# Performance work log

Measured on AMD Instinct MI355X. Metric: run time of the kernel, lower is better.

## Reference

```python
import jax, jax.numpy as jnp
import numpy as np

EMB = 16
N_LEFT = 100000
N_RIGHT = 100000
N_EDGES = 3200000


def setup_inputs() -> dict:
    key = jax.random.key(0)
    ks = jax.random.split(key, 16)
    s = 1.0 / np.sqrt(EMB)
    inp = {
        "left_features": jax.random.normal(ks[0], (N_LEFT, EMB), jnp.float32),
        "edge_indices": jax.random.randint(ks[1], (2, N_EDGES), 0, N_RIGHT, jnp.int64) if jax.config.jax_enable_x64 else jax.random.randint(ks[1], (2, N_EDGES), 0, N_RIGHT, jnp.int32),
        "edge_features": jax.random.normal(ks[2], (N_EDGES, 1), jnp.float32),
        "right_features": jax.random.normal(ks[3], (N_RIGHT, EMB), jnp.float32),
        # feature_module_left: Linear(emb, emb, bias=True)
        "W_left": jax.random.uniform(ks[4], (EMB, EMB), jnp.float32, -s, s),
        "b_left": jax.random.uniform(ks[5], (EMB,), jnp.float32, -s, s),
        # feature_module_edge: Linear(1, emb, bias=False)
        "W_edge": jax.random.uniform(ks[6], (1, EMB), jnp.float32, -1.0, 1.0),
        # feature_module_right: Linear(emb, emb, bias=False)
        "W_right": jax.random.uniform(ks[7], (EMB, EMB), jnp.float32, -s, s),
        # feature_module_final: ReLU -> Linear(emb, emb)
        "W_final": jax.random.uniform(ks[8], (EMB, EMB), jnp.float32, -s, s),
        "b_final": jax.random.uniform(ks[9], (EMB,), jnp.float32, -s, s),
        # post_conv_module: ReLU -> Linear(emb, emb)
        "W_post": jax.random.uniform(ks[10], (EMB, EMB), jnp.float32, -s, s),
        "b_post": jax.random.uniform(ks[11], (EMB,), jnp.float32, -s, s),
        # output_module: Linear(2*emb, emb) -> ReLU -> Linear(emb, emb)
        "W_out1": jax.random.uniform(ks[12], (2 * EMB, EMB), jnp.float32, -1.0 / np.sqrt(2 * EMB), 1.0 / np.sqrt(2 * EMB)),
        "b_out1": jax.random.uniform(ks[13], (EMB,), jnp.float32, -s, s),
        "W_out2": jax.random.uniform(ks[14], (EMB, EMB), jnp.float32, -s, s),
        "b_out2": jax.random.uniform(ks[15], (EMB,), jnp.float32, -s, s),
    }
    return inp


def reference(left_features, edge_indices, edge_features, right_features,
              W_left, b_left, W_edge, W_right, W_final, b_final,
              W_post, b_post, W_out1, b_out1, W_out2, b_out2):
    left_idx = edge_indices[0]
    right_idx = edge_indices[1]
    n_right = right_features.shape[0]

    # per-edge messages: [E, emb]
    msg_left = left_features[left_idx] @ W_left + b_left
    msg_edge = edge_features @ W_edge
    msg_right = right_features[right_idx] @ W_right
    messages = jax.nn.relu(msg_left + msg_edge + msg_right) @ W_final + b_final

    # scatter-add over right nodes
    aggregated = jax.ops.segment_sum(messages, right_idx, num_segments=n_right)

    post = jax.nn.relu(aggregated) @ W_post + b_post
    h = jnp.concatenate([post, right_features], axis=-1)  # [N_right, 2*emb]
    out = jax.nn.relu(h @ W_out1 + b_out1) @ W_out2 + b_out2
    return out
```

## Files before the change

### kernel.cpp

```cpp
#include <hip/hip_runtime.h>

#define EMB 16
#define NPB 196
#define BNODES 256
#define MAXNB 512
#define PCHUNK 6656
#define RPTC 13
#define MAXCHUNKS 512
#define REC_CAP 2048
#define RPT 4
typedef unsigned int u32;
typedef unsigned long long u64;

__global__ void zero_f32(float* __restrict__ p, size_t n) {
    size_t i = (size_t)blockIdx.x * blockDim.x + threadIdx.x;
    size_t stride = (size_t)gridDim.x * blockDim.x;
    for (; i < n; i += stride) p[i] = 0.0f;
}

__global__ void zero_i32(int* __restrict__ p, int n) {
    int i = blockIdx.x * blockDim.x + threadIdx.x;
    if (i < n) p[i] = 0;
}

__device__ __forceinline__ u32 bf16bits_rne(float x) {
    u32 u = __float_as_uint(x);
    return (u + 0x7fffu + ((u >> 16) & 1u)) >> 16;
}

__global__ void linear16_pack_kernel(const float* __restrict__ X, const float* __restrict__ W,
                                     const float* __restrict__ b, u32* __restrict__ Y, int N) {
    int tid = blockIdx.x * blockDim.x + threadIdx.x;
    int row = tid >> 3;
    int h = tid & 7;
    if (row >= N) return;
    float a0 = b ? b[h] : 0.0f;
    float a1 = b ? b[h + 8] : 0.0f;
    const float* xr = X + (size_t)row * EMB;
#pragma unroll
    for (int k = 0; k < EMB; ++k) {
        float xv = xr[k];
        a0 = fmaf(xv, W[k * EMB + h], a0);
        a1 = fmaf(xv, W[k * EMB + h + 8], a1);
    }
    Y[(size_t)row * 8 + h] = (bf16bits_rne(a1) << 16) | bf16bits_rne(a0);
}

__global__ void linear16_kernel(const float* __restrict__ X, const float* __restrict__ W,
                                const float* __restrict__ b, float* __restrict__ Y, int N) {
    int tid = blockIdx.x * blockDim.x + threadIdx.x;
    int row = tid >> 4;
    int j = tid & 15;
    if (row >= N) return;
    float acc = b ? b[j] : 0.0f;
    const float* xr = X + (size_t)row * EMB;
#pragma unroll
    for (int k = 0; k < EMB; ++k) acc = fmaf(xr[k], W[k * EMB + j], acc);
    Y[(size_t)row * EMB + j] = acc;
}

__launch_bounds__(512)
__global__ void chunk_sort_kernel(const int* __restrict__ eidx, const float* __restrict__ ef,
                                  u64* __restrict__ rec, int* __restrict__ cntM,
                                  int* __restrict__ cbaseM, int E, int NB) {
    __shared__ u64 srec[PCHUNK];
    __shared__ int hist[MAXNB];
    __shared__ int wsum[8];
    int t = threadIdx.x;
    int lane = t & 63, wid = t >> 6;
    int c = blockIdx.x;
    long long base = (long long)c * PCHUNK;
    int n = (int)(((long long)E - base) < PCHUNK ? ((long long)E - base) : PCHUNK);
    const int* ridx = eidx + E;

    for (int i = t; i < NB; i += 512) hist[i] = 0;
    __syncthreads();
    u64 rcv[RPTC];
    int pk[RPTC];
#pragma unroll
    for (int k = 0; k < RPTC; ++k) {
        int i = t + k * 512;
        rcv[k] = 0; pk[k] = 0;
        if (i < n) {
            int r = ridx[base + i];
            int l = eidx[base + i];
            float f = ef[base + i];
            int bb = r / NPB;
            int rl = r - bb * NPB;
            int rank = atomicAdd(&hist[bb], 1);
            rcv[k] = ((u64)__float_as_uint(f) << 32) | ((u64)(u32)l << 8) | (u32)rl;
            pk[k] = (bb << 13) | rank;
        }
    }
    __syncthreads();
    int v = (t < NB) ? hist[t] : 0;
    int inc = v;
#pragma unroll
    for (int d = 1; d < 64; d <<= 1) {
        int x = __shfl_up(inc, d, 64);
        if (lane >= d) inc += x;
    }
    if (lane == 63) wsum[wid] = inc;
    __syncthreads();
    int off = 0;
#pragma unroll
    for (int w = 0; w < 8; ++w) off += (w < wid) ? wsum[w] : 0;
    int ex = off + inc - v;
    if (t < NB) {
        cntM[(size_t)c * NB + t] = v;
        cbaseM[(size_t)c * NB + t] = ex;
        hist[t] = ex;
    }
    __syncthreads();
#pragma unroll
    for (int k = 0; k < RPTC; ++k) {
        int i = t + k * 512;
        if (i < n) srec[hist[pk[k] >> 13] + (pk[k] & 8191)] = rcv[k];
    }
    __syncthreads();
    for (int i = t; i < n; i += 512) rec[base + i] = srec[i];
}

__launch_bounds__(512)
__global__ void bucket_gather_kernel(const u64* __restrict__ rec, const int* __restrict__ cntM,
                                     const int* __restrict__ cbaseM,
                                     const u32* __restrict__ Lpk, const u32* __restrict__ Rpk,
                                     const float* __restrict__ We, const float* __restrict__ rf,
                                     const float* __restrict__ Wf, const float* __restrict__ bf,
                                     const float* __restrict__ Wp, const float* __restrict__ bp,
                                     const float* __restrict__ Wo1, const float* __restrict__ bo1,
                                     const float* __restrict__ Wo2, const float* __restrict__ bo2,
                                     float* __restrict__ out,
                                     int n_right, int NB, int nchunks) {
    __shared__ u64 srec[REC_CAP];
    __shared__ u32 addrtab[REC_CAP];
    __shared__ int runsum[MAXCHUNKS + 1];
    __shared__ int rbase[MAXCHUNKS];
    __shared__ int hist[BNODES], base_[BNODES];
    __shared__ int wsum[8];
    __shared__ float sWf[256], sWp[256], sWo1[512], sWo2[256], sb[64];
    int b = blockIdx.x;
    int t = threadIdx.x;
    int lane = t & 63, wid = t >> 6;
    int node0 = b * NPB;

    if (t < 256) { sWf[t] = Wf[t]; sWp[t] = Wp[t]; sWo2[t] = Wo2[t]; }
    sWo1[t] = Wo1[t];
    if (t < 16) { sb[t] = bf[t]; sb[16 + t] = bp[t]; sb[32 + t] = bo1[t]; sb[48 + t] = bo2[t]; }

    int len = (t < nchunks) ? cntM[(size_t)t * NB + b] : 0;
    int inc = len;
#pragma unroll
    for (int d = 1; d < 64; d <<= 1) {
        int x = __shfl_up(inc, d, 64);
        if (lane >= d) inc += x;
    }
    if (lane == 63) wsum[wid] = inc;
    __syncthreads();
    int off = 0;
#pragma unroll
    for (int w = 0; w < 8; ++w) off += (w < wid) ? wsum[w] : 0;
    int pexcl = off + inc - len;
    if (t < nchunks) { runsum[t] = pexcl; rbase[t] = t * PCHUNK + cbaseM[(size_t)t * NB + b]; }
    if (t == 511) runsum[nchunks] = off + inc;
    __syncthreads();
    int total = runsum[nchunks];

    int n = t >> 1, q = t & 1;
    int node = node0 + n;
    bool nv = (n < NPB) && (node < n_right);

    float we[16];
#pragma unroll
    for (int j = 0; j < 16; ++j) we[j] = We[j];

    float rv[16];
    if (nv) {
        const uint4* rp = (const uint4*)(Rpk + (size_t)node * 8);
        uint4 ra = rp[0], rb = rp[1];
        u32 w0 = ra.x, w1 = ra.y, w2 = ra.z, w3 = ra.w;
        u32 w4 = rb.x, w5 = rb.y, w6 = rb.z, w7 = rb.w;
        rv[0] = __uint_as_float(w0 << 16); rv[8]  = __uint_as_float(w0 & 0xffff0000u);
        rv[1] = __uint_as_float(w1 << 16); rv[9]  = __uint_as_float(w1 & 0xffff0000u);
        rv[2] = __uint_as_float(w2 << 16); rv[10] = __uint_as_float(w2 & 0xffff0000u);
        rv[3] = __uint_as_float(w3 << 16); rv[11] = __uint_as_float(w3 & 0xffff0000u);
        rv[4] = __uint_as_float(w4 << 16); rv[12] = __uint_as_float(w4 & 0xffff0000u);
        rv[5] = __uint_as_float(w5 << 16); rv[13] = __uint_as_float(w5 & 0xffff0000u);
        rv[6] = __uint_as_float(w6 << 16); rv[14] = __uint_as_float(w6 & 0xffff0000u);
        rv[7] = __uint_as_float(w7 << 16); rv[15] = __uint_as_float(w7 & 0xffff0000u);
    } else {
#pragma unroll
        for (int j = 0; j < 16; ++j) rv[j] = 0.0f;
    }

    float acc[16];
#pragma unroll
    for (int j = 0; j < 16; ++j) acc[j] = 0.0f;
    int dsum = 0;

    for (int tile0 = 0; tile0 < total; tile0 += REC_CAP) {
        int m = total - tile0; if (m > REC_CAP) m = REC_CAP;
        u64 rcl[RPT];
        int rnk[RPT];
        if (t < BNODES) hist[t] = 0;
        for (int r = t; r < nchunks; r += 512) {
            int g_lo = runsum[r], g_hi = runsum[r + 1];
            int lo = g_lo > tile0 ? g_lo : tile0;
            int hi = g_hi < tile0 + m ? g_hi : tile0 + m;
            int a = rbase[r] + (lo - g_lo);
            for (int g = lo; g < hi; ++g, ++a) addrtab[g - tile0] = (u32)a;
        }
        __syncthreads();
#pragma unroll
        for (int k = 0; k < RPT; ++k) {
            int i = t + k * 512;
            rcl[k] = (i < m) ? rec[(size_t)addrtab[i]] : 0;
        }
#pragma unroll
        for (int k = 0; k < RPT; ++k) {
            int i = t + k * 512;
            rnk[k] = (i < m) ? atomicAdd(&hist[(int)(rcl[k] & 0xffu)], 1) : 0;
        }
        __syncthreads();
        if (t < 64) {
            int h0 = hist[4 * t], h1 = hist[4 * t + 1], h2 = hist[4 * t + 2], h3 = hist[4 * t + 3];
            int s4 = h0 + h1 + h2 + h3;
            int inc4 = s4;
#pragma unroll
            for (int d = 1; d < 64; d <<= 1) {
                int x = __shfl_up(inc4, d, 64);
                if (t >= d) inc4 += x;
            }
            int ex = inc4 - s4;
            base_[4 * t] = ex;
            base_[4 * t + 1] = ex + h0;
            base_[4 * t + 2] = ex + h0 + h1;
            base_[4 * t + 3] = ex + h0 + h1 + h2;
        }
        __syncthreads();
#pragma unroll
        for (int k = 0; k < RPT; ++k) {
            int i = t + k * 512;
            if (i < m) srec[base_[(int)(rcl[k] & 0xffu)] + rnk[k]] = rcl[k];
        }
        __syncthreads();
        {
            int cc = nv ? hist[n] : 0;
            int b0_ = nv ? base_[n] : 0;
            if (q == 0) dsum += cc;
            for (int k = q; k < cc; k += 2) {
                u64 rc = srec[b0_ + k];
                int l = (int)((rc >> 8) & 0xFFFFFFu);
                float f = __uint_as_float((u32)(rc >> 32));
                const uint4* lp = (const uint4*)(Lpk + (size_t)l * 8);
                uint4 la = lp[0], lb = lp[1];
                u32 w0 = la.x, w1 = la.y, w2 = la.z, w3 = la.w;
                u32 w4 = lb.x, w5 = lb.y, w6 = lb.z, w7 = lb.w;
#define PAIR(h, lw) { \
                float l0 = __uint_as_float(lw << 16); \
                float l1 = __uint_as_float(lw & 0xffff0000u); \
                acc[h]     += fmaxf(fmaf(f, we[h], l0) + rv[h], 0.0f); \
                acc[h + 8] += fmaxf(fmaf(f, we[h + 8], l1) + rv[h + 8], 0.0f); }
                PAIR(0, w0) PAIR(1, w1) PAIR(2, w2) PAIR(3, w3)
                PAIR(4, w4) PAIR(5, w5) PAIR(6, w6) PAIR(7, w7)
#undef PAIR
            }
        }
        __syncthreads();
    }

#pragma unroll
    for (int j = 0; j < 16; ++j) acc[j] += __shfl_xor(acc[j], 1, 64);
    dsum += __shfl_xor(dsum, 1, 64);

    if (nv) {
        float rfx[16];
        const float4* Rf = (const float4*)(rf + (size_t)node * EMB);
#pragma unroll
        for (int k = 0; k < 4; ++k) {
            float4 w = Rf[k];
            rfx[4 * k] = w.x; rfx[4 * k + 1] = w.y; rfx[4 * k + 2] = w.z; rfx[4 * k + 3] = w.w;
        }
        float c = (float)dsum;
        float x[16], y[16], z[16], o[16];
#pragma unroll
        for (int j = 0; j < 16; ++j) {
            float a = c * sb[j];
#pragma unroll
            for (int k = 0; k < 16; ++k) a = fmaf(acc[k], sWf[k * 16 + j], a);
            x[j] = fmaxf(a, 0.0f);
        }
#pragma unroll
        for (int j = 0; j < 16; ++j) {
            float a = sb[16 + j];
#pragma unroll
            for (int k = 0; k < 16; ++k) a = fmaf(x[k], sWp[k * 16 + j], a);
            y[j] = a;
        }
#pragma unroll
        for (int j = 0; j < 16; ++j) {
            float a = sb[32 + j];
#pragma unroll
            for (int k = 0; k < 16; ++k) a = fmaf(y[k], sWo1[k * 16 + j], a);
#pragma unroll
            for (int k = 0; k < 16; ++k) a = fmaf(rfx[k], sWo1[(16 + k) * 16 + j], a);
            z[j] = fmaxf(a, 0.0f);
        }
#pragma unroll
        for (int j = 0; j < 16; ++j) {
            float a = sb[48 + j];
#pragma unroll
            for (int k = 0; k < 16; ++k) a = fmaf(z[k], sWo2[k * 16 + j], a);
            o[j] = a;
        }
        float4* Op = (float4*)(out + (size_t)node * EMB);
        Op[q * 2]     = make_float4(o[q * 8],     o[q * 8 + 1], o[q * 8 + 2], o[q * 8 + 3]);
        Op[q * 2 + 1] = make_float4(o[q * 8 + 4], o[q * 8 + 5], o[q * 8 + 6], o[q * 8 + 7]);
    }
}

__global__ void edge_kernel(const int* __restrict__ eidx, const float* __restrict__ ef,
                            const float* __restrict__ L, const float* __restrict__ R,
                            const float* __restrict__ We, float* __restrict__ S,
                            int* __restrict__ cnt, int E) {
    long long tid = (long long)blockIdx.x * blockDim.x + threadIdx.x;
    int e = (int)(tid >> 4);
    int j = (int)(tid & 15);
    if (e >= E) return;
    int l = eidx[e];
    int r = eidx[E + e];
    float v = L[(size_t)l * EMB + j] + ef[e] * We[j] + R[(size_t)r * EMB + j];
    v = fmaxf(v, 0.0f);
    unsafeAtomicAdd(&S[(size_t)r * EMB + j], v);
    if (j == 0) atomicAdd(&cnt[r], 1);
}

__global__ void final_kernel(const float* __restrict__ S, const int* __restrict__ deg,
                             const float* __restrict__ rf,
                             const float* __restrict__ Wf, const float* __restrict__ bf,
                             const float* __restrict__ Wp, const float* __restrict__ bp,
                             const float* __restrict__ Wo1, const float* __restrict__ bo1,
                             const float* __restrict__ Wo2, const float* __restrict__ bo2,
                             float* __restrict__ out, int N) {
    __shared__ float sWf[256], sWp[256], sWo1[512], sWo2[256];
    __shared__ float sb[64];
    int t = threadIdx.x;
    for (int i = t; i < 256; i += 256) { sWf[i] = Wf[i]; sWp[i] = Wp[i]; sWo2[i] = Wo2[i]; }
    for (int i = t; i < 512; i += 256) sWo1[i] = Wo1[i];
    if (t < 16) { sb[t] = bf[t]; sb[16 + t] = bp[t]; sb[32 + t] = bo1[t]; sb[48 + t] = bo2[t]; }
    __syncthreads();

    int r = blockIdx.x * blockDim.x + t;
    if (r >= N) return;

    float s[16], x[16], y[16], rv[16], z[16], o[16];
    const float4* Sp = (const float4*)(S + (size_t)r * EMB);
    const float4* Rp = (const float4*)(rf + (size_t)r * EMB);
#pragma unroll
    for (int k = 0; k < 4; ++k) {
        float4 v = Sp[k];
        s[4 * k] = v.x; s[4 * k + 1] = v.y; s[4 * k + 2] = v.z; s[4 * k + 3] = v.w;
        float4 w = Rp[k];
        rv[4 * k] = w.x; rv[4 * k + 1] = w.y; rv[4 * k + 2] = w.z; rv[4 * k + 3] = w.w;
    }
    float c = (float)deg[r];

#pragma unroll
    for (int j = 0; j < 16; ++j) {
        float a = c * sb[j];
#pragma unroll
        for (int k = 0; k < 16; ++k) a = fmaf(s[k], sWf[k * 16 + j], a);
        x[j] = fmaxf(a, 0.0f);
    }
#pragma unroll
    for (int j = 0; j < 16; ++j) {
        float a = sb[16 + j];
#pragma unroll
        for (int k = 0; k < 16; ++k) a = fmaf(x[k], sWp[k * 16 + j], a);
        y[j] = a;
    }
#pragma unroll
    for (int j = 0; j < 16; ++j) {
        float a = sb[32 + j];
#pragma unroll
        for (int k = 0; k < 16; ++k) a = fmaf(y[k], sWo1[k * 16 + j], a);
#pragma unroll
        for (int k = 0; k < 16; ++k) a = fmaf(rv[k], sWo1[(16 + k) * 16 + j], a);
        z[j] = fmaxf(a, 0.0f);
    }
#pragma unroll
    for (int j = 0; j < 16; ++j) {
        float a = sb[48 + j];
#pragma unroll
        for (int k = 0; k < 16; ++k) a = fmaf(z[k], sWo2[k * 16 + j], a);
        o[j] = a;
    }
    float4* Op = (float4*)(out + (size_t)r * EMB);
#pragma unroll
    for (int k = 0; k < 4; ++k)
        Op[k] = make_float4(o[4 * k], o[4 * k + 1], o[4 * k + 2], o[4 * k + 3]);
}

extern "C" void kernel_launch(void* const* d_in, const int* in_sizes, int n_in,
                              void* d_out, int out_size, void* d_ws, size_t ws_size,
                              hipStream_t stream) {
    const float* lf     = (const float*)d_in[0];
    const int*   eidx   = (const int*)d_in[1];
    const float* ef     = (const float*)d_in[2];
    const float* rf     = (const float*)d_in[3];
    const float* W_left = (const float*)d_in[4];
    const float* b_left = (const float*)d_in[5];
    const float* W_edge = (const float*)d_in[6];
    const float* W_right= (const float*)d_in[7];
    const float* W_final= (const float*)d_in[8];
    const float* b_final= (const float*)d_in[9];
    const float* W_post = (const float*)d_in[10];
    const float* b_post = (const float*)d_in[11];
    const float* W_out1 = (const float*)d_in[12];
    const float* b_out1 = (const float*)d_in[13];
    const float* W_out2 = (const float*)d_in[14];
    const float* b_out2 = (const float*)d_in[15];

    int n_left  = in_sizes[0] / EMB;
    int E       = in_sizes[2];
    int n_right = in_sizes[3] / EMB;
    float* out = (float*)d_out;

    int NB = (n_right + NPB - 1) / NPB;
    int nchunks = (E + PCHUNK - 1) / PCHUNK;

    size_t need = (size_t)E * 8
                + (size_t)nchunks * NB * 8
                + ((size_t)n_left + n_right) * 32;

    if (ws_size >= need && NB <= MAXNB && nchunks <= MAXCHUNKS) {
        u64* rec    = (u64*)d_ws;
        int* cntM   = (int*)(rec + (size_t)E);
        int* cbaseM = cntM + (size_t)nchunks * NB;
        u32* Lpk    = (u32*)(cbaseM + (size_t)nchunks * NB);
        u32* Rpk    = Lpk + (size_t)n_left * 8;

        linear16_pack_kernel<<<(n_left * 8 + 255) / 256, 256, 0, stream>>>(lf, W_left, b_left, Lpk, n_left);
        linear16_pack_kernel<<<(n_right * 8 + 255) / 256, 256, 0, stream>>>(rf, W_right, nullptr, Rpk, n_right);

        chunk_sort_kernel<<<nchunks, 512, 0, stream>>>(eidx, ef, rec, cntM, cbaseM, E, NB);

        bucket_gather_kernel<<<NB, 512, 0, stream>>>(rec, cntM, cbaseM, Lpk, Rpk, W_edge, rf,
                                                     W_final, b_final, W_post, b_post,
                                                     W_out1, b_out1, W_out2, b_out2,
                                                     out, n_right, NB, nchunks);
    } else {
        float* L   = (float*)d_ws;
        float* R   = L + (size_t)n_left * EMB;
        float* S   = R + (size_t)n_right * EMB;
        int*   cnt = (int*)(S + (size_t)n_right * EMB);

        zero_f32<<<2048, 256, 0, stream>>>(S, (size_t)n_right * EMB);
        zero_i32<<<(n_right + 255) / 256, 256, 0, stream>>>(cnt, n_right);

        linear16_kernel<<<(n_left * EMB + 255) / 256, 256, 0, stream>>>(lf, W_left, b_left, L, n_left);
        linear16_kernel<<<(n_right * EMB + 255) / 256, 256, 0, stream>>>(rf, W_right, nullptr, R, n_right);

        long long ethreads = (long long)E * EMB;
        edge_kernel<<<(unsigned)((ethreads + 255) / 256), 256, 0, stream>>>(eidx, ef, L, R, W_edge, S, cnt, E);

        final_kernel<<<(n_right + 255) / 256, 256, 0, stream>>>(S, cnt, rf,
            W_final, b_final, W_post, b_post, W_out1, b_out1, W_out2, b_out2, out, n_right);
    }
}
```

Baseline: 86.35 us.

## Halve nodes per bucket, use four threads per node, transpose chunk metadata

Buckets shrink from 196 to 98 right nodes, so the gather kernel launches about twice as many blocks (about 1021) and each node's edges are split across four threads instead of two, reduced with an extra xor shuffle. The chunk sort now scans two buckets per thread and writes count and base as a single int2 in bucket-major order, so each gather block reads its per-chunk metadata contiguously instead of with a stride. The aim is more parallelism in the gather and cheaper metadata reads. The cost is twice as much metadata written and each block doing the same per-chunk address-table setup over half as many edges.

```diff
diff --git a/kernel.cpp b/kernel.cpp
--- a/kernel.cpp
+++ b/kernel.cpp
@@ -1,9 +1,9 @@
 #include <hip/hip_runtime.h>
 
 #define EMB 16
-#define NPB 196
-#define BNODES 256
-#define MAXNB 512
+#define NPB 98
+#define NHIST 128
+#define MAXNB 1024
 #define PCHUNK 6656
 #define RPTC 13
 #define MAXCHUNKS 512
@@ -61,8 +61,8 @@
 
 __launch_bounds__(512)
 __global__ void chunk_sort_kernel(const int* __restrict__ eidx, const float* __restrict__ ef,
-                                  u64* __restrict__ rec, int* __restrict__ cntM,
-                                  int* __restrict__ cbaseM, int E, int NB) {
+                                  u64* __restrict__ rec, int2* __restrict__ cbM,
+                                  int E, int NB, int nchunks) {
     __shared__ u64 srec[PCHUNK];
     __shared__ int hist[MAXNB];
     __shared__ int wsum[8];
@@ -93,8 +93,11 @@
         }
     }
     __syncthreads();
-    int v = (t < NB) ? hist[t] : 0;
-    int inc = v;
+    int b0 = 2 * t, b1 = 2 * t + 1;
+    int v0 = (b0 < NB) ? hist[b0] : 0;
+    int v1 = (b1 < NB) ? hist[b1] : 0;
+    int s2 = v0 + v1;
+    int inc = s2;
 #pragma unroll
     for (int d = 1; d < 64; d <<= 1) {
         int x = __shfl_up(inc, d, 64);
@@ -105,12 +108,9 @@
     int off = 0;
 #pragma unroll
     for (int w = 0; w < 8; ++w) off += (w < wid) ? wsum[w] : 0;
-    int ex = off + inc - v;
-    if (t < NB) {
-        cntM[(size_t)c * NB + t] = v;
-        cbaseM[(size_t)c * NB + t] = ex;
-        hist[t] = ex;
-    }
+    int ex = off + inc - s2;
+    if (b0 < NB) { cbM[(size_t)b0 * nchunks + c] = make_int2(v0, ex);      hist[b0] = ex; }
+    if (b1 < NB) { cbM[(size_t)b1 * nchunks + c] = make_int2(v1, ex + v0); hist[b1] = ex + v0; }
     __syncthreads();
 #pragma unroll
     for (int k = 0; k < RPTC; ++k) {
@@ -122,8 +122,7 @@
 }
 
 __launch_bounds__(512)
-__global__ void bucket_gather_kernel(const u64* __restrict__ rec, const int* __restrict__ cntM,
-                                     const int* __restrict__ cbaseM,
+__global__ void bucket_gather_kernel(const u64* __restrict__ rec, const int2* __restrict__ cbM,
                                      const u32* __restrict__ Lpk, const u32* __restrict__ Rpk,
                                      const float* __restrict__ We, const float* __restrict__ rf,
                                      const float* __restrict__ Wf, const float* __restrict__ bf,
@@ -136,7 +135,7 @@
     __shared__ u32 addrtab[REC_CAP];
     __shared__ int runsum[MAXCHUNKS + 1];
     __shared__ int rbase[MAXCHUNKS];
-    __shared__ int hist[BNODES], base_[BNODES];
+    __shared__ int hist[NHIST], base_[NHIST];
     __shared__ int wsum[8];
     __shared__ float sWf[256], sWp[256], sWo1[512], sWo2[256], sb[64];
     int b = blockIdx.x;
@@ -148,7 +147,8 @@
     sWo1[t] = Wo1[t];
     if (t < 16) { sb[t] = bf[t]; sb[16 + t] = bp[t]; sb[32 + t] = bo1[t]; sb[48 + t] = bo2[t]; }
 
-    int len = (t < nchunks) ? cntM[(size_t)t * NB + b] : 0;
+    int len = 0, cb = 0;
+    if (t < nchunks) { int2 v = cbM[(size_t)b * nchunks + t]; len = v.x; cb = v.y; }
     int inc = len;
 #pragma unroll
     for (int d = 1; d < 64; d <<= 1) {
@@ -161,12 +161,12 @@
 #pragma unroll
     for (int w = 0; w < 8; ++w) off += (w < wid) ? wsum[w] : 0;
     int pexcl = off + inc - len;
-    if (t < nchunks) { runsum[t] = pexcl; rbase[t] = t * PCHUNK + cbaseM[(size_t)t * NB + b]; }
+    if (t < nchunks) { runsum[t] = pexcl; rbase[t] = t * PCHUNK + cb; }
     if (t == 511) runsum[nchunks] = off + inc;
     __syncthreads();
     int total = runsum[nchunks];
 
-    int n = t >> 1, q = t & 1;
+    int n = t >> 2, q = t & 3;
     int node = node0 + n;
     bool nv = (n < NPB) && (node < n_right);
 
@@ -202,7 +202,7 @@
         int m = total - tile0; if (m > REC_CAP) m = REC_CAP;
         u64 rcl[RPT];
         int rnk[RPT];
-        if (t < BNODES) hist[t] = 0;
+        if (t < NHIST) hist[t] = 0;
         for (int r = t; r < nchunks; r += 512) {
             int g_lo = runsum[r], g_hi = runsum[r + 1];
             int lo = g_lo > tile0 ? g_lo : tile0;
@@ -223,19 +223,17 @@
         }
         __syncthreads();
         if (t < 64) {
-            int h0 = hist[4 * t], h1 = hist[4 * t + 1], h2 = hist[4 * t + 2], h3 = hist[4 * t + 3];
-            int s4 = h0 + h1 + h2 + h3;
-            int inc4 = s4;
+            int h0 = hist[2 * t], h1 = hist[2 * t + 1];
+            int s2 = h0 + h1;
+            int inc2 = s2;
 #pragma unroll
             for (int d = 1; d < 64; d <<= 1) {
-                int x = __shfl_up(inc4, d, 64);
-                if (t >= d) inc4 += x;
+                int x = __shfl_up(inc2, d, 64);
+                if (t >= d) inc2 += x;
             }
-            int ex = inc4 - s4;
-            base_[4 * t] = ex;
-            base_[4 * t + 1] = ex + h0;
-            base_[4 * t + 2] = ex + h0 + h1;
-            base_[4 * t + 3] = ex + h0 + h1 + h2;
+            int ex = inc2 - s2;
+            base_[2 * t] = ex;
+            base_[2 * t + 1] = ex + h0;
         }
         __syncthreads();
 #pragma unroll
@@ -248,7 +246,7 @@
             int cc = nv ? hist[n] : 0;
             int b0_ = nv ? base_[n] : 0;
             if (q == 0) dsum += cc;
-            for (int k = q; k < cc; k += 2) {
+            for (int k = q; k < cc; k += 4) {
                 u64 rc = srec[b0_ + k];
                 int l = (int)((rc >> 8) & 0xFFFFFFu);
                 float f = __uint_as_float((u32)(rc >> 32));
@@ -270,8 +268,12 @@
     }
 
 #pragma unroll
-    for (int j = 0; j < 16; ++j) acc[j] += __shfl_xor(acc[j], 1, 64);
+    for (int j = 0; j < 16; ++j) {
+        acc[j] += __shfl_xor(acc[j], 1, 64);
+        acc[j] += __shfl_xor(acc[j], 2, 64);
+    }
     dsum += __shfl_xor(dsum, 1, 64);
+    dsum += __shfl_xor(dsum, 2, 64);
 
     if (nv) {
         float rfx[16];
@@ -314,8 +316,7 @@
             o[j] = a;
         }
         float4* Op = (float4*)(out + (size_t)node * EMB);
-        Op[q * 2]     = make_float4(o[q * 8],     o[q * 8 + 1], o[q * 8 + 2], o[q * 8 + 3]);
-        Op[q * 2 + 1] = make_float4(o[q * 8 + 4], o[q * 8 + 5], o[q * 8 + 6], o[q * 8 + 7]);
+        Op[q] = make_float4(o[q * 4], o[q * 4 + 1], o[q * 4 + 2], o[q * 4 + 3]);
     }
 }
 
@@ -430,22 +431,21 @@
     int nchunks = (E + PCHUNK - 1) / PCHUNK;
 
     size_t need = (size_t)E * 8
-                + (size_t)nchunks * NB * 8
+                + (size_t)NB * nchunks * 8
                 + ((size_t)n_left + n_right) * 32;
 
     if (ws_size >= need && NB <= MAXNB && nchunks <= MAXCHUNKS) {
-        u64* rec    = (u64*)d_ws;
-        int* cntM   = (int*)(rec + (size_t)E);
-        int* cbaseM = cntM + (size_t)nchunks * NB;
-        u32* Lpk    = (u32*)(cbaseM + (size_t)nchunks * NB);
-        u32* Rpk    = Lpk + (size_t)n_left * 8;
+        u64*  rec = (u64*)d_ws;
+        int2* cbM = (int2*)(rec + (size_t)E);
+        u32*  Lpk = (u32*)(cbM + (size_t)NB * nchunks);
+        u32*  Rpk = Lpk + (size_t)n_left * 8;
 
         linear16_pack_kernel<<<(n_left * 8 + 255) / 256, 256, 0, stream>>>(lf, W_left, b_left, Lpk, n_left);
         linear16_pack_kernel<<<(n_right * 8 + 255) / 256, 256, 0, stream>>>(rf, W_right, nullptr, Rpk, n_right);
 
-        chunk_sort_kernel<<<nchunks, 512, 0, stream>>>(eidx, ef, rec, cntM, cbaseM, E, NB);
-
-        bucket_gather_kernel<<<NB, 512, 0, stream>>>(rec, cntM, cbaseM, Lpk, Rpk, W_edge, rf,
+        chunk_sort_kernel<<<nchunks, 512, 0, stream>>>(eidx, ef, rec, cbM, E, NB, nchunks);
+
+        bucket_gather_kernel<<<NB, 512, 0, stream>>>(rec, cbM, Lpk, Rpk, W_edge, rf,
                                                      W_final, b_final, W_post, b_post,
                                                      W_out1, b_out1, W_out2, b_out2,
                                                      out, n_right, NB, nchunks);
```

New measurement: 104.9 us. +21.5%, slower.
